# Performance work log

Hardware: AMD Instinct MI355X
Metric: run time of the kernel (lower is better)

Reference implementation:

```python
import jax, jax.numpy as jnp
import numpy as np
import itertools, math

D_K, K_BITS, L_TABLES, M_ENS = 64, 4, 8, 2
B_SZ, T_LEN, H_HEADS = 2, 512, 8


def setup_inputs() -> dict:
    key = jax.random.key(0)
    k1, k2, k3, k4 = jax.random.split(key, 4)
    shape = (M_ENS, B_SZ, T_LEN, H_HEADS, D_K)
    Khf = jax.random.normal(k1, shape, dtype=jnp.float32)
    Vhf = jax.random.normal(k2, shape, dtype=jnp.float32)
    Qhf = jax.random.normal(k3, shape, dtype=jnp.float32)
    # shared random hyperplanes: [L, K, d_k] -> [d_k, L*K]
    planes = jax.random.normal(k4, (L_TABLES, K_BITS, D_K), dtype=jnp.float32)
    planes_T = planes.reshape(L_TABLES * K_BITS, D_K).T
    # hypercube corners: [R, K] -> [K, R], R = 2**K
    corners = np.array(list(itertools.product([-1.0, 1.0], repeat=K_BITS)), dtype=np.float32)
    protos_T = jnp.asarray(corners.T)
    return {"Khf": Khf, "Vhf": Vhf, "Qhf": Qhf, "planes_T": planes_T, "protos_T": protos_T}


def reference(Khf, Vhf, Qhf, planes_T, protos_T):
    M, B, T, H, dk = Khf.shape
    K = protos_T.shape[0]
    L = planes_T.shape[1] // K
    scale = math.sqrt(dk)
    N = M * B * H

    # [M,B,T,H,dk] -> [N,T,dk] with N = M*B*H (heads folded next to batch)
    def fold(x):
        return jnp.transpose(x, (0, 1, 3, 2, 4)).reshape(N, T, dk)

    Kh2, Qh2, V2 = fold(Khf), fold(Qhf), fold(Vhf)

    # random-hyperplane projections -> per-table softmax over 2**K corners
    def probs(x):
        proj = (x @ planes_T).reshape(N, T, L, K)          # [N,T,L,K]
        logits = jnp.einsum('ntlk,kr->ntlr', jnp.tanh(proj) / scale, protos_T)
        return jax.nn.softmax(logits, axis=-1)             # [N,T,L,R]

    probsK = probs(Kh2)
    probsQ = probs(Qh2)

    # causal prefix sums (linear-attention style state)
    A_pref = jnp.cumsum(probsK, axis=1)                    # [N,T,L,R]
    B_pref = jnp.cumsum(probsK[..., None] * V2[:, :, None, None, :], axis=1)  # [N,T,L,R,dk]
    E_pref = B_pref / (A_pref[..., None] + 1e-6)

    out2 = jnp.einsum('ntlr,ntlrd->ntd', probsQ, E_pref)   # [N,T,dk]
    out = out2.reshape(M, B, H, T, dk).transpose(0, 1, 3, 2, 4)
    return out
```

## Files before the change

kernel.cpp:

```cpp
#include <hip/hip_runtime.h>
#include <hip/hip_bf16.h>
#include <math.h>

#define T_LEN 512
#define H_HEADS 8
#define DK 64
#define LR 128
#define NTOT 32

typedef __attribute__((ext_vector_type(8))) short bf16x8;
typedef __attribute__((ext_vector_type(4))) float f32x4;

__device__ __forceinline__ float fast_tanh(float x) {
    float e = __expf(2.0f * x);
    return 1.0f - 2.0f / (1.0f + e);
}

__device__ __forceinline__ unsigned f2bf(float x) {
    union { float f; unsigned u; } v; v.f = x;
    unsigned r = v.u + 0x7FFF + ((v.u >> 16) & 1);
    return r >> 16;
}

__device__ __forceinline__ float bflo(unsigned u) {
    union { unsigned u; float f; } v; v.u = u << 16; return v.f;
}
__device__ __forceinline__ float bfhi(unsigned u) {
    union { unsigned u; float f; } v; v.u = u & 0xFFFF0000u; return v.f;
}

__global__ __launch_bounds__(256) void k_probs(
    const float* __restrict__ Khf, const float* __restrict__ Qhf,
    const float* __restrict__ Vhf,
    const float* __restrict__ planesT, const float* __restrict__ protosT,
    unsigned short* __restrict__ pKB, unsigned short* __restrict__ pKt,
    unsigned short* __restrict__ pQB, unsigned short* __restrict__ VBT,
    float* __restrict__ Spart)
{
    __shared__ __align__(16) unsigned char smraw[39424];
    short* Psh    = (short*)smraw;
    float* protos = (float*)(smraw + 4608);
    short* Xsh    = (short*)(smraw + 4864);
    float* xt     = (float*)(smraw + 14080);
    float* pbuf   = (float*)(smraw + 22528);
    float* vb     = xt;

    const int bx = blockIdx.x;
    const int n  = bx >> 4;
    const int tile = bx & 15;
    const int t0 = tile * 32;
    const int g  = n >> 3, h = n & 7;
    const int tid = threadIdx.x;
    const int wv = tid >> 6, lane = tid & 63, m16 = lane & 15, q = lane >> 4;

    {
        int d = tid >> 2, jb = (tid & 3) * 8;
        float4 a = *(const float4*)(planesT + d * 32 + jb);
        float4 b = *(const float4*)(planesT + d * 32 + jb + 4);
        float pv[8] = {a.x, a.y, a.z, a.w, b.x, b.y, b.z, b.w};
#pragma unroll
        for (int i = 0; i < 8; ++i)
            Psh[(jb + i) * 72 + d] = (short)f2bf(pv[i]);
    }
    if (tid < 64) protos[tid] = protosT[tid];
#pragma unroll
    for (int it = 0; it < 2; ++it) {
        int vid = it * 256 + tid;
        int row = vid >> 3, seg = vid & 7;
        const float* src = (row < 32 ? Khf : Qhf) +
            ((long)(g * T_LEN + t0 + (row & 31)) * H_HEADS + h) * DK + seg * 8;
        float4 a = *(const float4*)src;
        float4 b = *(const float4*)(src + 4);
        uint4 u;
        u.x = f2bf(a.x) | (f2bf(a.y) << 16);
        u.y = f2bf(a.z) | (f2bf(a.w) << 16);
        u.z = f2bf(b.x) | (f2bf(b.y) << 16);
        u.w = f2bf(b.z) | (f2bf(b.w) << 16);
        *(uint4*)(Xsh + row * 72 + seg * 8) = u;
    }
    __syncthreads();

    {
        f32x4 s[2];
        s[0] = s[1] = (f32x4){0.f, 0.f, 0.f, 0.f};
#pragma unroll
        for (int ks = 0; ks < 2; ++ks) {
            bf16x8 af = *(const bf16x8*)(Xsh + (wv * 16 + m16) * 72 + ks * 32 + q * 8);
#pragma unroll
            for (int nb = 0; nb < 2; ++nb) {
                bf16x8 bf = *(const bf16x8*)(Psh + (nb * 16 + m16) * 72 + ks * 32 + q * 8);
                s[nb] = __builtin_amdgcn_mfma_f32_16x16x32_bf16(af, bf, s[nb], 0, 0, 0);
            }
        }
#pragma unroll
        for (int nb = 0; nb < 2; ++nb)
#pragma unroll
            for (int p = 0; p < 4; ++p)
                xt[(wv * 16 + q * 4 + p) * 33 + nb * 16 + m16] =
                    fast_tanh(s[nb][p]) * 0.125f;
    }
    __syncthreads();

    const int r = tid & 15, l = (tid >> 4) & 7, thi = tid >> 7;
    for (int side = 0; side < 2; ++side) {
        float p0 = protos[r], p1 = protos[16 + r], p2 = protos[32 + r], p3 = protos[48 + r];
#pragma unroll 4
        for (int w = 0; w < 16; ++w) {
            int tl = w * 2 + thi;
            const float* x = xt + (side * 32 + tl) * 33 + l * 4;
            float logit = x[0] * p0 + x[1] * p1 + x[2] * p2 + x[3] * p3;
            float e = __expf(logit);
            float s = e;
            s += __shfl_xor(s, 1, 16);
            s += __shfl_xor(s, 2, 16);
            s += __shfl_xor(s, 4, 16);
            s += __shfl_xor(s, 8, 16);
            pbuf[(l * 16 + r) * 33 + tl] = e / s;
        }
        __syncthreads();
        unsigned* dst = (unsigned*)(side ? pQB : pKB);
#pragma unroll
        for (int it = 0; it < 8; ++it) {
            int fid = it * 256 + tid;
            int lr = fid >> 4, tp2 = fid & 15;
            unsigned u0 = f2bf(pbuf[lr * 33 + tp2 * 2]);
            unsigned u1 = f2bf(pbuf[lr * 33 + tp2 * 2 + 1]);
            dst[(size_t)(n * LR + lr) * 256 + tile * 16 + tp2] = u0 | (u1 << 16);
        }
        if (side == 0) {
            unsigned* dt = (unsigned*)pKt + (size_t)n * 32768 + t0 * 64;
#pragma unroll
            for (int it = 0; it < 8; ++it) {
                int fid = it * 256 + tid;
                int t = fid >> 6, lrp = fid & 63;
                unsigned u0 = f2bf(pbuf[(2 * lrp) * 33 + t]);
                unsigned u1 = f2bf(pbuf[(2 * lrp + 1) * 33 + t]);
                dt[t * 64 + lrp] = u0 | (u1 << 16);
            }
            if (tid < 128) {
                float s = 0.f;
                const float* row = pbuf + tid * 33;
#pragma unroll 8
                for (int t = 0; t < 32; ++t) s += row[t];
                Spart[((size_t)n * 16 + tile) * 128 + tid] = s;
            }
        }
        __syncthreads();
    }

#pragma unroll
    for (int it = 0; it < 2; ++it) {
        int fid = it * 256 + tid;
        int t = fid >> 4, c4 = fid & 15;
        float4 v = *(const float4*)(Vhf + ((size_t)(g * T_LEN + t0 + t) * H_HEADS + h) * DK + c4 * 4);
        vb[(c4 * 4 + 0) * 33 + t] = v.x;
        vb[(c4 * 4 + 1) * 33 + t] = v.y;
        vb[(c4 * 4 + 2) * 33 + t] = v.z;
        vb[(c4 * 4 + 3) * 33 + t] = v.w;
    }
    __syncthreads();
    {
        unsigned* dstv = (unsigned*)VBT + (size_t)n * 16384;
#pragma unroll
        for (int it = 0; it < 4; ++it) {
            int fid = it * 256 + tid;
            int d = fid >> 4, tp2 = fid & 15;
            unsigned u0 = f2bf(vb[d * 33 + tp2 * 2]);
            unsigned u1 = f2bf(vb[d * 33 + tp2 * 2 + 1]);
            dstv[d * 256 + tile * 16 + tp2] = u0 | (u1 << 16);
        }
    }
}

__global__ __launch_bounds__(1024) void k_attn(
    const unsigned short* __restrict__ pKB, const unsigned short* __restrict__ pKt,
    const unsigned short* __restrict__ pQB, const unsigned short* __restrict__ VBT,
    const float* __restrict__ Spart, float* __restrict__ out)
{
    __shared__ __align__(16) short sm[71680];
    const int n = blockIdx.x >> 3, rt = blockIdx.x & 7;
    const int g = n >> 3, h = n & 7;
    const int tid = threadIdx.x;
    const int wave = tid >> 6, wg = wave >> 2, w = wave & 3;
    const int lane = tid & 63, m16 = lane & 15, q = lane >> 4;
    const int gtid = tid & 255;

    short* Ksh = sm + wg * 8704;
    short* Vsh = sm + 34816 + wg * 4608;
    short* Ssh = sm + 53248 + wg * 4608;
    short* Qsh = sm;

    {
        const int s8 = lane & 7;
        const int lr = wave * 8 + (lane >> 3);
        float bsum = 0.f;
        for (int j = 0; j < 2 * rt; ++j)
            bsum += Spart[((size_t)n * 16 + j) * 128 + lr];
        uint4 ku = *(const uint4*)(pKB + ((size_t)n * LR + lr) * 512 + rt * 64 + s8 * 8);
        unsigned kuu[4] = {ku.x, ku.y, ku.z, ku.w};
        float s[8];
        s[0] = bflo(kuu[0]);        s[1] = s[0] + bfhi(kuu[0]);
        s[2] = s[1] + bflo(kuu[1]); s[3] = s[2] + bfhi(kuu[1]);
        s[4] = s[3] + bflo(kuu[2]); s[5] = s[4] + bfhi(kuu[2]);
        s[6] = s[5] + bflo(kuu[3]); s[7] = s[6] + bfhi(kuu[3]);
        float tot = s[7];
#pragma unroll
        for (int off = 1; off < 8; off <<= 1) {
            float v = __shfl_up(tot, off, 8);
            if (s8 >= off) tot += v;
        }
        float base = bsum + tot - s[7];
        uint4 qu = *(const uint4*)(pQB + ((size_t)n * LR + lr) * 512 + rt * 64 + s8 * 8);
        unsigned quu[4] = {qu.x, qu.y, qu.z, qu.w};
        float qf[8] = {bflo(quu[0]), bfhi(quu[0]), bflo(quu[1]), bfhi(quu[1]),
                       bflo(quu[2]), bfhi(quu[2]), bflo(quu[3]), bfhi(quu[3])};
        const int qbase = ((wave ^ s8) << 3) + (lr & 7);
#pragma unroll
        for (int i = 0; i < 8; ++i)
            Qsh[(s8 * 8 + i) * 136 + qbase] = (short)f2bf(qf[i] / (base + s[i] + 1e-6f));
    }
    __syncthreads();

    bf16x8 qa[4];
    {
        const int row = w * 16 + m16, rk = row >> 3;
#pragma unroll
        for (int st = 0; st < 4; ++st)
            qa[st] = *(const bf16x8*)(Qsh + row * 136 + (((st * 4 + q) ^ rk) << 3));
    }

    const unsigned short* kt = pKt + (size_t)n * 65536;
    const unsigned short* kv = VBT + (size_t)n * 32768;
    uint4 pk[4], pv[2];
    auto pref = [&](int c) {
#pragma unroll
        for (int it = 0; it < 4; ++it) {
            int fid = it * 256 + gtid;
            pk[it] = *(const uint4*)(kt + (size_t)(c * 64 + (fid >> 4)) * 128 + (fid & 15) * 8);
        }
#pragma unroll
        for (int it = 0; it < 2; ++it) {
            int fid = it * 256 + gtid;
            pv[it] = *(const uint4*)(kv + (size_t)(fid >> 3) * 512 + c * 64 + (fid & 7) * 8);
        }
    };

    f32x4 o[4];
    o[0] = o[1] = o[2] = o[3] = (f32x4){0.f, 0.f, 0.f, 0.f};

    if (wg <= rt) pref(wg);
    const int rounds = (rt >> 2) + 1;
    for (int r0 = 0; r0 < rounds; ++r0) {
        const int c = r0 * 4 + wg;
        const bool act = (c <= rt);
        __syncthreads();
        if (act) {
#pragma unroll
            for (int it = 0; it < 4; ++it) {
                int fid = it * 256 + gtid;
                *(uint4*)(Ksh + (fid >> 4) * 136 + (fid & 15) * 8) = pk[it];
            }
            *(uint4*)(Vsh + (gtid >> 3) * 72 + (gtid & 7) * 8) = pv[0];
            *(uint4*)(Vsh + ((gtid + 256) >> 3) * 72 + (gtid & 7) * 8) = pv[1];
        }
        __syncthreads();
        if (c + 4 <= rt) pref(c + 4);
        if (act) {
            f32x4 s[4];
            s[0] = s[1] = s[2] = s[3] = (f32x4){0.f, 0.f, 0.f, 0.f};
#pragma unroll
            for (int st = 0; st < 4; ++st)
#pragma unroll
                for (int nb = 0; nb < 4; ++nb) {
                    bf16x8 b = *(const bf16x8*)(Ksh + (nb * 16 + m16) * 136 + st * 32 + q * 8);
                    s[nb] = __builtin_amdgcn_mfma_f32_16x16x32_bf16(qa[st], b, s[nb], 0, 0, 0);
                }
            if (c == rt) {
#pragma unroll
                for (int nb = 0; nb < 4; ++nb)
#pragma unroll
                    for (int p = 0; p < 4; ++p)
                        if (nb * 16 + m16 > w * 16 + q * 4 + p) s[nb][p] = 0.f;
            }
#pragma unroll
            for (int nb = 0; nb < 4; ++nb)
#pragma unroll
                for (int p = 0; p < 4; ++p) {
                    union { float f; unsigned u; } cv; cv.f = s[nb][p];
                    Ssh[(w * 16 + q * 4 + p) * 72 + nb * 16 + m16] =
                        (short)((cv.u + 0x8000u) >> 16);
                }
#pragma unroll
            for (int st = 0; st < 2; ++st) {
                bf16x8 a = *(const bf16x8*)(Ssh + (w * 16 + m16) * 72 + st * 32 + q * 8);
#pragma unroll
                for (int nb = 0; nb < 4; ++nb) {
                    bf16x8 b = *(const bf16x8*)(Vsh + (nb * 16 + m16) * 72 + st * 32 + q * 8);
                    o[nb] = __builtin_amdgcn_mfma_f32_16x16x32_bf16(a, b, o[nb], 0, 0, 0);
                }
            }
        }
    }

    __syncthreads();
    float* Obuf = (float*)sm;
    if (wg) {
        float* ob = Obuf + (wg - 1) * 4352;
#pragma unroll
        for (int nb = 0; nb < 4; ++nb)
#pragma unroll
            for (int p = 0; p < 4; ++p)
                ob[(w * 16 + q * 4 + p) * 68 + nb * 16 + m16] = o[nb][p];
    }
    __syncthreads();
    if (wg == 0) {
        float* dst = out + ((size_t)(g * T_LEN + rt * 64 + w * 16 + q * 4) * H_HEADS + h) * DK;
#pragma unroll
        for (int p = 0; p < 4; ++p)
#pragma unroll
            for (int nb = 0; nb < 4; ++nb) {
                int idx = (w * 16 + q * 4 + p) * 68 + nb * 16 + m16;
                dst[p * (H_HEADS * DK) + nb * 16 + m16] =
                    o[nb][p] + Obuf[idx] + Obuf[4352 + idx] + Obuf[8704 + idx];
            }
    }
}

extern "C" void kernel_launch(void* const* d_in, const int* in_sizes, int n_in,
                              void* d_out, int out_size, void* d_ws, size_t ws_size,
                              hipStream_t stream) {
    const float* Khf     = (const float*)d_in[0];
    const float* Vhf     = (const float*)d_in[1];
    const float* Qhf     = (const float*)d_in[2];
    const float* planesT = (const float*)d_in[3];
    const float* protosT = (const float*)d_in[4];
    float* outp = (float*)d_out;

    const size_t NE = (size_t)NTOT * LR * T_LEN;
    unsigned short* pKB = (unsigned short*)d_ws;
    unsigned short* pKt = pKB + NE;
    unsigned short* pQB = pKt + NE;
    unsigned short* VBT = pQB + NE;
    float* Spart = (float*)(VBT + (size_t)NTOT * DK * T_LEN);

    k_probs<<<dim3(512), dim3(256), 0, stream>>>(
        Khf, Qhf, Vhf, planesT, protosT, pKB, pKt, pQB, VBT, Spart);
    k_attn<<<dim3(256), dim3(1024), 0, stream>>>(pKB, pKt, pQB, VBT, Spart, outp);
}
```

Before: 108.2 us.

## Split K and Q probability work into separate blocks and remap block indices

The probs kernel now launches twice as many blocks, each handling either the K side or the Q side (Q blocks also transpose V), instead of one block doing both sequentially. This shortens each block's critical path, removes a loop with extra barriers, and halves the per-block MFMA work to one tile per wave. Block index mapping in both kernels is changed so the head index varies fastest. The cost is duplicated plane/proto loading per block and somewhat uneven work between K and Q blocks.

```diff
diff --git a/kernel.cpp b/kernel.cpp
--- a/kernel.cpp
+++ b/kernel.cpp
@@ -37,17 +37,19 @@
     unsigned short* __restrict__ pQB, unsigned short* __restrict__ VBT,
     float* __restrict__ Spart)
 {
-    __shared__ __align__(16) unsigned char smraw[39424];
+    __shared__ __align__(16) unsigned char smraw[39040];
     short* Psh    = (short*)smraw;
     float* protos = (float*)(smraw + 4608);
     short* Xsh    = (short*)(smraw + 4864);
-    float* xt     = (float*)(smraw + 14080);
-    float* pbuf   = (float*)(smraw + 22528);
-    float* vb     = xt;
+    float* xt     = (float*)(smraw + 9472);
+    float* pbuf   = (float*)(smraw + 13696);
+    float* vb     = (float*)(smraw + 30592);
 
     const int bx = blockIdx.x;
-    const int n  = bx >> 4;
-    const int tile = bx & 15;
+    const int n  = bx & 31;
+    const int u  = bx >> 5;
+    const int tile = u >> 1;
+    const int side = u & 1;
     const int t0 = tile * 32;
     const int g  = n >> 3, h = n & 7;
     const int tid = threadIdx.x;
@@ -63,51 +65,44 @@
             Psh[(jb + i) * 72 + d] = (short)f2bf(pv[i]);
     }
     if (tid < 64) protos[tid] = protosT[tid];
-#pragma unroll
-    for (int it = 0; it < 2; ++it) {
-        int vid = it * 256 + tid;
-        int row = vid >> 3, seg = vid & 7;
-        const float* src = (row < 32 ? Khf : Qhf) +
-            ((long)(g * T_LEN + t0 + (row & 31)) * H_HEADS + h) * DK + seg * 8;
+    {
+        int row = tid >> 3, seg = tid & 7;
+        const float* src = (side ? Qhf : Khf) +
+            ((long)(g * T_LEN + t0 + row) * H_HEADS + h) * DK + seg * 8;
         float4 a = *(const float4*)src;
         float4 b = *(const float4*)(src + 4);
-        uint4 u;
-        u.x = f2bf(a.x) | (f2bf(a.y) << 16);
-        u.y = f2bf(a.z) | (f2bf(a.w) << 16);
-        u.z = f2bf(b.x) | (f2bf(b.y) << 16);
-        u.w = f2bf(b.z) | (f2bf(b.w) << 16);
-        *(uint4*)(Xsh + row * 72 + seg * 8) = u;
-    }
-    __syncthreads();
-
-    {
-        f32x4 s[2];
-        s[0] = s[1] = (f32x4){0.f, 0.f, 0.f, 0.f};
+        uint4 uu;
+        uu.x = f2bf(a.x) | (f2bf(a.y) << 16);
+        uu.y = f2bf(a.z) | (f2bf(a.w) << 16);
+        uu.z = f2bf(b.x) | (f2bf(b.y) << 16);
+        uu.w = f2bf(b.z) | (f2bf(b.w) << 16);
+        *(uint4*)(Xsh + row * 72 + seg * 8) = uu;
+    }
+    __syncthreads();
+
+    {
+        const int mb = wv & 1, nb = wv >> 1;
+        f32x4 s = (f32x4){0.f, 0.f, 0.f, 0.f};
 #pragma unroll
         for (int ks = 0; ks < 2; ++ks) {
-            bf16x8 af = *(const bf16x8*)(Xsh + (wv * 16 + m16) * 72 + ks * 32 + q * 8);
-#pragma unroll
-            for (int nb = 0; nb < 2; ++nb) {
-                bf16x8 bf = *(const bf16x8*)(Psh + (nb * 16 + m16) * 72 + ks * 32 + q * 8);
-                s[nb] = __builtin_amdgcn_mfma_f32_16x16x32_bf16(af, bf, s[nb], 0, 0, 0);
-            }
-        }
-#pragma unroll
-        for (int nb = 0; nb < 2; ++nb)
-#pragma unroll
-            for (int p = 0; p < 4; ++p)
-                xt[(wv * 16 + q * 4 + p) * 33 + nb * 16 + m16] =
-                    fast_tanh(s[nb][p]) * 0.125f;
+            bf16x8 af = *(const bf16x8*)(Xsh + (mb * 16 + m16) * 72 + ks * 32 + q * 8);
+            bf16x8 bf = *(const bf16x8*)(Psh + (nb * 16 + m16) * 72 + ks * 32 + q * 8);
+            s = __builtin_amdgcn_mfma_f32_16x16x32_bf16(af, bf, s, 0, 0, 0);
+        }
+#pragma unroll
+        for (int p = 0; p < 4; ++p)
+            xt[(mb * 16 + q * 4 + p) * 33 + nb * 16 + m16] =
+                fast_tanh(s[p]) * 0.125f;
     }
     __syncthreads();
 
     const int r = tid & 15, l = (tid >> 4) & 7, thi = tid >> 7;
-    for (int side = 0; side < 2; ++side) {
+    {
         float p0 = protos[r], p1 = protos[16 + r], p2 = protos[32 + r], p3 = protos[48 + r];
 #pragma unroll 4
         for (int w = 0; w < 16; ++w) {
             int tl = w * 2 + thi;
-            const float* x = xt + (side * 32 + tl) * 33 + l * 4;
+            const float* x = xt + tl * 33 + l * 4;
             float logit = x[0] * p0 + x[1] * p1 + x[2] * p2 + x[3] * p3;
             float e = __expf(logit);
             float s = e;
@@ -117,8 +112,23 @@
             s += __shfl_xor(s, 8, 16);
             pbuf[(l * 16 + r) * 33 + tl] = e / s;
         }
-        __syncthreads();
-        unsigned* dst = (unsigned*)(side ? pQB : pKB);
+    }
+    if (side) {
+#pragma unroll
+        for (int it = 0; it < 2; ++it) {
+            int fid = it * 256 + tid;
+            int t = fid >> 4, c4 = fid & 15;
+            float4 v = *(const float4*)(Vhf + ((size_t)(g * T_LEN + t0 + t) * H_HEADS + h) * DK + c4 * 4);
+            vb[(c4 * 4 + 0) * 33 + t] = v.x;
+            vb[(c4 * 4 + 1) * 33 + t] = v.y;
+            vb[(c4 * 4 + 2) * 33 + t] = v.z;
+            vb[(c4 * 4 + 3) * 33 + t] = v.w;
+        }
+    }
+    __syncthreads();
+
+    if (side == 0) {
+        unsigned* dst = (unsigned*)pKB;
 #pragma unroll
         for (int it = 0; it < 8; ++it) {
             int fid = it * 256 + tid;
@@ -127,39 +137,34 @@
             unsigned u1 = f2bf(pbuf[lr * 33 + tp2 * 2 + 1]);
             dst[(size_t)(n * LR + lr) * 256 + tile * 16 + tp2] = u0 | (u1 << 16);
         }
-        if (side == 0) {
-            unsigned* dt = (unsigned*)pKt + (size_t)n * 32768 + t0 * 64;
-#pragma unroll
-            for (int it = 0; it < 8; ++it) {
-                int fid = it * 256 + tid;
-                int t = fid >> 6, lrp = fid & 63;
-                unsigned u0 = f2bf(pbuf[(2 * lrp) * 33 + t]);
-                unsigned u1 = f2bf(pbuf[(2 * lrp + 1) * 33 + t]);
-                dt[t * 64 + lrp] = u0 | (u1 << 16);
-            }
-            if (tid < 128) {
-                float s = 0.f;
-                const float* row = pbuf + tid * 33;
-#pragma unroll 8
-                for (int t = 0; t < 32; ++t) s += row[t];
-                Spart[((size_t)n * 16 + tile) * 128 + tid] = s;
-            }
-        }
-        __syncthreads();
-    }
-
-#pragma unroll
-    for (int it = 0; it < 2; ++it) {
-        int fid = it * 256 + tid;
-        int t = fid >> 4, c4 = fid & 15;
-        float4 v = *(const float4*)(Vhf + ((size_t)(g * T_LEN + t0 + t) * H_HEADS + h) * DK + c4 * 4);
-        vb[(c4 * 4 + 0) * 33 + t] = v.x;
-        vb[(c4 * 4 + 1) * 33 + t] = v.y;
-        vb[(c4 * 4 + 2) * 33 + t] = v.z;
-        vb[(c4 * 4 + 3) * 33 + t] = v.w;
-    }
-    __syncthreads();
-    {
+        unsigned* dt = (unsigned*)pKt + (size_t)n * 32768 + t0 * 64;
+#pragma unroll
+        for (int it = 0; it < 8; ++it) {
+            int fid = it * 256 + tid;
+            int t = fid >> 6, lrp = fid & 63;
+            unsigned u0 = f2bf(pbuf[(2 * lrp) * 33 + t]);
+            unsigned u1 = f2bf(pbuf[(2 * lrp + 1) * 33 + t]);
+            dt[t * 64 + lrp] = u0 | (u1 << 16);
+        }
+        {
+            int lr = tid >> 1, hf = tid & 1;
+            float s = 0.f;
+            const float* row = pbuf + lr * 33 + hf * 16;
+#pragma unroll
+            for (int t = 0; t < 16; ++t) s += row[t];
+            s += __shfl_xor(s, 1, 2);
+            if (!hf) Spart[((size_t)n * 16 + tile) * 128 + lr] = s;
+        }
+    } else {
+        unsigned* dst = (unsigned*)pQB;
+#pragma unroll
+        for (int it = 0; it < 8; ++it) {
+            int fid = it * 256 + tid;
+            int lr = fid >> 4, tp2 = fid & 15;
+            unsigned u0 = f2bf(pbuf[lr * 33 + tp2 * 2]);
+            unsigned u1 = f2bf(pbuf[lr * 33 + tp2 * 2 + 1]);
+            dst[(size_t)(n * LR + lr) * 256 + tile * 16 + tp2] = u0 | (u1 << 16);
+        }
         unsigned* dstv = (unsigned*)VBT + (size_t)n * 16384;
 #pragma unroll
         for (int it = 0; it < 4; ++it) {
@@ -178,7 +183,7 @@
     const float* __restrict__ Spart, float* __restrict__ out)
 {
     __shared__ __align__(16) short sm[71680];
-    const int n = blockIdx.x >> 3, rt = blockIdx.x & 7;
+    const int n = blockIdx.x & 31, rt = blockIdx.x >> 5;
     const int g = n >> 3, h = n & 7;
     const int tid = threadIdx.x;
     const int wave = tid >> 6, wg = wave >> 2, w = wave & 3;
@@ -343,7 +348,7 @@
     unsigned short* VBT = pQB + NE;
     float* Spart = (float*)(VBT + (size_t)NTOT * DK * T_LEN);
 
-    k_probs<<<dim3(512), dim3(256), 0, stream>>>(
+    k_probs<<<dim3(1024), dim3(256), 0, stream>>>(
         Khf, Qhf, Vhf, planesT, protosT, pKB, pKt, pQB, VBT, Spart);
     k_attn<<<dim3(256), dim3(1024), 0, stream>>>(pKB, pKt, pQB, VBT, Spart, outp);
 }
```

Result: faster. 102.9 us (-4.9%).
